# Performance work log

Measured on AMD Instinct MI355X. Metric: run time of the kernel, lower is better.

The kernel has to match this reference:

```python
import jax, jax.numpy as jnp
import numpy as np

N_NODES, N_LAYERS, D = 4096, 8, 128


def setup_inputs() -> dict:
    key = jax.random.key(0)
    k1, k2, k3 = jax.random.split(key, 3)
    feature = jax.random.normal(k1, (N_NODES, N_LAYERS, D), dtype=jnp.float32)
    W = jax.random.uniform(k2, (D, D), dtype=jnp.float32)
    adj = jax.random.randint(k3, (N_LAYERS, N_NODES, N_NODES), 0, 2, dtype=jnp.int32)
    return {"feature": feature, "W": W, "adj": adj}


def reference(feature, W, adj):
    # feature: [N, L, D]; W: [D, D]; adj: [L, N, N] with 0/1 entries.
    # Original loop: for i, for l, for j in neighbors(i) U {i}:
    #     ret[j, l, :] = (W @ feature[i, l, :]) / sqrt(d_i * d_j)   # OVERWRITE
    # => final ret[j, l] uses the LAST source i with adj[l,i,j]==1 or i==j.
    L, N = adj.shape[0], adj.shape[1]
    i_idx = jnp.arange(N)
    # mask[l, i, j]: source i writes to destination j at layer l
    mask = (adj == 1) | (i_idx[:, None] == i_idx[None, :])
    # last (largest) source index per (l, j); diagonal guarantees >= 0
    src = jnp.max(jnp.where(mask, i_idx[:, None], -1), axis=1)          # [L, N]
    deg = jnp.sum(adj, axis=2).astype(feature.dtype) + 1.0              # [L, N]
    # shared tiny GEMM applied to all (node, layer) features
    Wf = jnp.einsum('de,nle->lnd', W, feature)                          # [L, N, D]
    gathered = jnp.take_along_axis(Wf, src[:, :, None], axis=1)         # [L, N, D]
    d_src = jnp.take_along_axis(deg, src, axis=1)                       # [L, N]
    scale = 1.0 / jnp.sqrt(d_src * deg)                                 # [L, N]
    ret = jnp.transpose(gathered * scale[:, :, None], (1, 0, 2))        # [N, L, D]
    return ret
```

## Files before the change

kernel.cpp:

```cpp
#include <hip/hip_runtime.h>
#include <cstddef>

#define NN 4096
#define NL 8
#define ND 128

#define CHUNK 64
#define BATCH 16

typedef int   int4v   __attribute__((ext_vector_type(4)));
typedef float float4v __attribute__((ext_vector_type(4)));

__global__ __launch_bounds__(512, 4) void fused_kernel(
    const float* __restrict__ feature, const float* __restrict__ W,
    const int* __restrict__ adj, float* __restrict__ out) {
  __shared__ int      s_cand[32][CHUNK];
  __shared__ int      s_src[CHUNK];
  __shared__ int      s_found[CHUNK];
  __shared__ unsigned s_mask[NN / 32];
  __shared__ int      s_ps[NN / 32];
  __shared__ int      s_list[CHUNK];
  __shared__ int      s_smap[CHUNK];
  __shared__ float    s_scj[CHUNK];
  __shared__ float    s_deg[2 * CHUNK];
  __shared__ float    s_fb[BATCH][ND];
  __shared__ float    s_wf[BATCH][ND];

  const int t = threadIdx.x;
  const int l = blockIdx.y;
  const int jbase = blockIdx.x * CHUNK;
  const int* __restrict__ Al = adj + (size_t)l * NN * NN;

  if (t < CHUNK) { s_src[t] = jbase + t; s_found[t] = 0; }
  if (t < NN / 32) s_mask[t] = 0u;
  __syncthreads();

  const int rw = t >> 4;
  const int cq = t & 15;
  int itop = NN - 1;
  for (;;) {
    const int i = itop - rw;
    int4v a = {0, 0, 0, 0};
    if (i > jbase)
      a = *reinterpret_cast<const int4v*>(Al + (size_t)i * NN + jbase + cq * 4);
    int4v c;
    c.x = (a.x != 0 && i > jbase + cq * 4 + 0) ? i : -1;
    c.y = (a.y != 0 && i > jbase + cq * 4 + 1) ? i : -1;
    c.z = (a.z != 0 && i > jbase + cq * 4 + 2) ? i : -1;
    c.w = (a.w != 0 && i > jbase + cq * 4 + 3) ? i : -1;
    *reinterpret_cast<int4v*>(&s_cand[rw][cq * 4]) = c;
    __syncthreads();
    bool mydone = true;
    if (t < CHUNK) {
      if (!s_found[t]) {
        int best = -1;
#pragma unroll
        for (int k = 0; k < 32; ++k) best = max(best, s_cand[k][t]);
        if (best >= 0) { s_src[t] = best; s_found[t] = 1; }
      }
      mydone = s_found[t] || (itop - 32 <= jbase + t);
    }
    itop -= 32;
    if (__syncthreads_and((int)mydone) || itop < 0) break;
  }

  if (t < CHUNK) atomicOr(&s_mask[s_src[t] >> 5], 1u << (s_src[t] & 31));
  __syncthreads();
  int pc = 0;
  if (t < 128) { pc = __popc(s_mask[t]); s_ps[t] = pc; }
  __syncthreads();
  for (int off = 1; off < 128; off <<= 1) {
    int v = 0;
    if (t < 128 && t >= off) v = s_ps[t - off];
    __syncthreads();
    if (t < 128 && t >= off) s_ps[t] += v;
    __syncthreads();
  }
  if (t < 128) {
    unsigned m = s_mask[t];
    int pos = s_ps[t] - pc;
    while (m) {
      int b = __ffs(m) - 1;
      m &= m - 1;
      s_list[pos++] = (t << 5) | b;
    }
  }
  __syncthreads();
  const int cnt = s_ps[127];
  if (t < CHUNK) {
    const int v = s_src[t], w = v >> 5;
    const int base = (w > 0) ? s_ps[w - 1] : 0;
    s_smap[t] = base + __popc(s_mask[w] & ((1u << (v & 31)) - 1));
  }

  const int wv = t >> 6;
  const int lane = t & 63;
  for (int r = wv; r < CHUNK; r += 8) {
    const int row = jbase + r;
    const int4v* __restrict__ p =
        reinterpret_cast<const int4v*>(Al + (size_t)row * NN);
    int s = 0;
    if (row & 1) {
#pragma unroll
      for (int k = 0; k < 16; ++k) {
        int4v v = __builtin_nontemporal_load(&p[lane + k * 64]);
        s += v.x + v.y + v.z + v.w;
      }
    } else {
#pragma unroll
      for (int k = 0; k < 16; ++k) {
        int4v v = p[lane + k * 64];
        s += v.x + v.y + v.z + v.w;
      }
    }
    for (int off = 32; off > 0; off >>= 1) s += __shfl_down(s, off, 64);
    if (lane == 0) s_deg[r] = (float)s + 1.0f;
  }
  for (int r = wv; r < cnt; r += 8) {
    const int4v* __restrict__ p =
        reinterpret_cast<const int4v*>(Al + (size_t)s_list[r] * NN);
    int s = 0;
#pragma unroll
    for (int k = 0; k < 16; ++k) {
      int4v v = p[lane + k * 64];
      s += v.x + v.y + v.z + v.w;
    }
    for (int off = 32; off > 0; off >>= 1) s += __shfl_down(s, off, 64);
    if (lane == 0) s_deg[CHUNK + r] = (float)s + 1.0f;
  }
  __syncthreads();
  if (t < CHUNK)
    s_scj[t] = rsqrtf(s_deg[t] * s_deg[CHUNK + s_smap[t]]);

  const int d = t & 127;
  const int quarter = t >> 7;
  const float4v* __restrict__ Wd =
      reinterpret_cast<const float4v*>(W + (size_t)d * ND);

  for (int b0 = 0; b0 < cnt; b0 += BATCH) {
    const int nb = min(BATCH, cnt - b0);
    {
      const int k = t >> 5, q = t & 31;
      if (k < nb)
        reinterpret_cast<float4v*>(s_fb[k])[q] =
            reinterpret_cast<const float4v*>(
                feature + ((size_t)s_list[b0 + k] * NL + l) * ND)[q];
    }
    __syncthreads();

#pragma unroll
    for (int kk = 0; kk < 4; ++kk) {
      const int k = quarter * 4 + kk;
      if (k < nb) {
        float4v a4 = {0.f, 0.f, 0.f, 0.f};
#pragma unroll
        for (int q = 0; q < 32; ++q)
          a4 += Wd[q] * reinterpret_cast<const float4v*>(s_fb[k])[q];
        s_wf[k][d] = a4.x + a4.y + a4.z + a4.w;
      }
    }
    __syncthreads();

    for (int idx = t; idx < CHUNK * 32; idx += 512) {
      const int r = idx >> 5, q = idx & 31;
      const int sl = s_smap[r] - b0;
      if (sl >= 0 && sl < nb) {
        const float sc = s_scj[r];
        float4v v = reinterpret_cast<const float4v*>(s_wf[sl])[q];
        v.x *= sc; v.y *= sc; v.z *= sc; v.w *= sc;
        __builtin_nontemporal_store(
            v, reinterpret_cast<float4v*>(out) +
                   ((size_t)(jbase + r) * NL + l) * 32 + q);
      }
    }
    __syncthreads();
  }
}

extern "C" void kernel_launch(void* const* d_in, const int* in_sizes, int n_in,
                              void* d_out, int out_size, void* d_ws,
                              size_t ws_size, hipStream_t stream) {
  const float* feature = (const float*)d_in[0];
  const float* W       = (const float*)d_in[1];
  const int*   adj     = (const int*)d_in[2];
  float* out = (float*)d_out;

  fused_kernel<<<dim3(NN / CHUNK, NL), 512, 0, stream>>>(feature, W, adj, out);
}
```

Measured before the change: 113.0 us.

## Overlap source search with degree row sums via warp specialization

Doubles the destination chunk per block and splits the block's waves into roles. Seven waves compute destination-row degree sums. The eighth wave alone scans the adjacency columns top-down with scalar loads to find the last source, builds the compacted source list with a wave-level scan, sums the source rows' degrees, and preloads the first feature batch. The goal is to hide the serialized search and its many block barriers behind the bandwidth-bound row-sum reads. The cost is that one wave now does the search and all source-row sums serially with strided scalar loads, and grid parallelism is halved.

```diff
diff --git a/kernel.cpp b/kernel.cpp
--- a/kernel.cpp
+++ b/kernel.cpp
@@ -5,18 +5,16 @@
 #define NL 8
 #define ND 128
 
-#define CHUNK 64
+#define CHUNK 128
 #define BATCH 16
 
 typedef int   int4v   __attribute__((ext_vector_type(4)));
 typedef float float4v __attribute__((ext_vector_type(4)));
 
-__global__ __launch_bounds__(512, 4) void fused_kernel(
+__global__ __launch_bounds__(512, 2) void fused_kernel(
     const float* __restrict__ feature, const float* __restrict__ W,
     const int* __restrict__ adj, float* __restrict__ out) {
-  __shared__ int      s_cand[32][CHUNK];
   __shared__ int      s_src[CHUNK];
-  __shared__ int      s_found[CHUNK];
   __shared__ unsigned s_mask[NN / 32];
   __shared__ int      s_ps[NN / 32];
   __shared__ int      s_list[CHUNK];
@@ -30,105 +28,125 @@
   const int l = blockIdx.y;
   const int jbase = blockIdx.x * CHUNK;
   const int* __restrict__ Al = adj + (size_t)l * NN * NN;
-
-  if (t < CHUNK) { s_src[t] = jbase + t; s_found[t] = 0; }
-  if (t < NN / 32) s_mask[t] = 0u;
-  __syncthreads();
-
-  const int rw = t >> 4;
-  const int cq = t & 15;
-  int itop = NN - 1;
-  for (;;) {
-    const int i = itop - rw;
-    int4v a = {0, 0, 0, 0};
-    if (i > jbase)
-      a = *reinterpret_cast<const int4v*>(Al + (size_t)i * NN + jbase + cq * 4);
-    int4v c;
-    c.x = (a.x != 0 && i > jbase + cq * 4 + 0) ? i : -1;
-    c.y = (a.y != 0 && i > jbase + cq * 4 + 1) ? i : -1;
-    c.z = (a.z != 0 && i > jbase + cq * 4 + 2) ? i : -1;
-    c.w = (a.w != 0 && i > jbase + cq * 4 + 3) ? i : -1;
-    *reinterpret_cast<int4v*>(&s_cand[rw][cq * 4]) = c;
-    __syncthreads();
-    bool mydone = true;
-    if (t < CHUNK) {
-      if (!s_found[t]) {
-        int best = -1;
-#pragma unroll
-        for (int k = 0; k < 32; ++k) best = max(best, s_cand[k][t]);
-        if (best >= 0) { s_src[t] = best; s_found[t] = 1; }
-      }
-      mydone = s_found[t] || (itop - 32 <= jbase + t);
-    }
-    itop -= 32;
-    if (__syncthreads_and((int)mydone) || itop < 0) break;
-  }
-
-  if (t < CHUNK) atomicOr(&s_mask[s_src[t] >> 5], 1u << (s_src[t] & 31));
-  __syncthreads();
-  int pc = 0;
-  if (t < 128) { pc = __popc(s_mask[t]); s_ps[t] = pc; }
-  __syncthreads();
-  for (int off = 1; off < 128; off <<= 1) {
-    int v = 0;
-    if (t < 128 && t >= off) v = s_ps[t - off];
-    __syncthreads();
-    if (t < 128 && t >= off) s_ps[t] += v;
-    __syncthreads();
-  }
-  if (t < 128) {
-    unsigned m = s_mask[t];
-    int pos = s_ps[t] - pc;
-    while (m) {
-      int b = __ffs(m) - 1;
-      m &= m - 1;
-      s_list[pos++] = (t << 5) | b;
-    }
-  }
-  __syncthreads();
-  const int cnt = s_ps[127];
-  if (t < CHUNK) {
-    const int v = s_src[t], w = v >> 5;
-    const int base = (w > 0) ? s_ps[w - 1] : 0;
-    s_smap[t] = base + __popc(s_mask[w] & ((1u << (v & 31)) - 1));
-  }
-
   const int wv = t >> 6;
   const int lane = t & 63;
-  for (int r = wv; r < CHUNK; r += 8) {
-    const int row = jbase + r;
-    const int4v* __restrict__ p =
-        reinterpret_cast<const int4v*>(Al + (size_t)row * NN);
-    int s = 0;
-    if (row & 1) {
-#pragma unroll
-      for (int k = 0; k < 16; ++k) {
-        int4v v = __builtin_nontemporal_load(&p[lane + k * 64]);
-        s += v.x + v.y + v.z + v.w;
-      }
-    } else {
+
+  if (wv < 7) {
+    for (int r = wv; r < CHUNK; r += 7) {
+      const int row = jbase + r;
+      const int4v* __restrict__ p =
+          reinterpret_cast<const int4v*>(Al + (size_t)row * NN);
+      int s = 0;
+      if (row & 1) {
+#pragma unroll
+        for (int k = 0; k < 16; ++k) {
+          int4v v = __builtin_nontemporal_load(&p[lane + k * 64]);
+          s += v.x + v.y + v.z + v.w;
+        }
+      } else {
+#pragma unroll
+        for (int k = 0; k < 16; ++k) {
+          int4v v = p[lane + k * 64];
+          s += v.x + v.y + v.z + v.w;
+        }
+      }
+      for (int off = 32; off > 0; off >>= 1) s += __shfl_down(s, off, 64);
+      if (lane == 0) s_deg[r] = (float)s + 1.0f;
+    }
+  } else {
+    const int j0 = jbase + lane;
+    const int j1 = jbase + 64 + lane;
+    int src0 = j0, src1 = j1;
+    bool f0 = false, f1 = false;
+    int itop = NN - 1;
+    for (;;) {
+      int a0[8], a1[8];
+#pragma unroll
+      for (int r = 0; r < 8; ++r) {
+        const int i = itop - r;
+        a0[r] = (i > j0) ? Al[(size_t)i * NN + j0] : 0;
+        a1[r] = (i > j1) ? Al[(size_t)i * NN + j1] : 0;
+      }
+#pragma unroll
+      for (int r = 0; r < 8; ++r) {
+        const int i = itop - r;
+        if (!f0 && a0[r] != 0 && i > j0) { src0 = i; f0 = true; }
+        if (!f1 && a1[r] != 0 && i > j1) { src1 = i; f1 = true; }
+      }
+      itop -= 8;
+      if (__all((f0 || itop <= j0) && (f1 || itop <= j1))) break;
+    }
+    s_src[lane] = src0;
+    s_src[lane + 64] = src1;
+    s_mask[2 * lane] = 0u;
+    s_mask[2 * lane + 1] = 0u;
+    __threadfence_block();
+    atomicOr(&s_mask[src0 >> 5], 1u << (src0 & 31));
+    atomicOr(&s_mask[src1 >> 5], 1u << (src1 & 31));
+    __threadfence_block();
+
+    const unsigned m0 = s_mask[2 * lane];
+    const unsigned m1 = s_mask[2 * lane + 1];
+    const int c = __popc(m0) + __popc(m1);
+    int sc = c;
+    for (int off = 1; off < 64; off <<= 1) {
+      int v = __shfl_up(sc, off, 64);
+      if (lane >= off) sc += v;
+    }
+    const int excl = sc - c;
+    const int ps0 = excl + __popc(m0);
+    s_ps[2 * lane] = ps0;
+    s_ps[2 * lane + 1] = ps0 + __popc(m1);
+    int pos = excl;
+    unsigned mm = m0;
+    while (mm) {
+      const int b = __ffs(mm) - 1;
+      mm &= mm - 1;
+      s_list[pos++] = ((2 * lane) << 5) | b;
+    }
+    mm = m1;
+    while (mm) {
+      const int b = __ffs(mm) - 1;
+      mm &= mm - 1;
+      s_list[pos++] = ((2 * lane + 1) << 5) | b;
+    }
+    const int cnt = __shfl(sc, 63, 64);
+    __threadfence_block();
+    {
+      const int v = src0, w = v >> 5;
+      const int base = (w > 0) ? s_ps[w - 1] : 0;
+      s_smap[lane] = base + __popc(s_mask[w] & ((1u << (v & 31)) - 1));
+    }
+    {
+      const int v = src1, w = v >> 5;
+      const int base = (w > 0) ? s_ps[w - 1] : 0;
+      s_smap[lane + 64] = base + __popc(s_mask[w] & ((1u << (v & 31)) - 1));
+    }
+    __threadfence_block();
+    for (int r = 0; r < cnt; ++r) {
+      const int4v* __restrict__ p =
+          reinterpret_cast<const int4v*>(Al + (size_t)s_list[r] * NN);
+      int s = 0;
 #pragma unroll
       for (int k = 0; k < 16; ++k) {
         int4v v = p[lane + k * 64];
         s += v.x + v.y + v.z + v.w;
       }
-    }
-    for (int off = 32; off > 0; off >>= 1) s += __shfl_down(s, off, 64);
-    if (lane == 0) s_deg[r] = (float)s + 1.0f;
-  }
-  for (int r = wv; r < cnt; r += 8) {
-    const int4v* __restrict__ p =
-        reinterpret_cast<const int4v*>(Al + (size_t)s_list[r] * NN);
-    int s = 0;
-#pragma unroll
-    for (int k = 0; k < 16; ++k) {
-      int4v v = p[lane + k * 64];
-      s += v.x + v.y + v.z + v.w;
-    }
-    for (int off = 32; off > 0; off >>= 1) s += __shfl_down(s, off, 64);
-    if (lane == 0) s_deg[CHUNK + r] = (float)s + 1.0f;
+      for (int off = 32; off > 0; off >>= 1) s += __shfl_down(s, off, 64);
+      if (lane == 0) s_deg[CHUNK + r] = (float)s + 1.0f;
+    }
+    const int nb0 = min(cnt, BATCH);
+    for (int idx = lane; idx < nb0 * 32; idx += 64) {
+      const int k = idx >> 5, q = idx & 31;
+      reinterpret_cast<float4v*>(s_fb[k])[q] =
+          reinterpret_cast<const float4v*>(
+              feature + ((size_t)s_list[k] * NL + l) * ND)[q];
+    }
   }
   __syncthreads();
+
+  const int cnt = s_ps[127];
+  const int nb0 = min(cnt, BATCH);
   if (t < CHUNK)
     s_scj[t] = rsqrtf(s_deg[t] * s_deg[CHUNK + s_smap[t]]);
 
@@ -136,18 +154,42 @@
   const int quarter = t >> 7;
   const float4v* __restrict__ Wd =
       reinterpret_cast<const float4v*>(W + (size_t)d * ND);
-
-  for (int b0 = 0; b0 < cnt; b0 += BATCH) {
+#pragma unroll
+  for (int kk = 0; kk < 4; ++kk) {
+    const int k = quarter * 4 + kk;
+    if (k < nb0) {
+      float4v a4 = {0.f, 0.f, 0.f, 0.f};
+#pragma unroll
+      for (int q = 0; q < 32; ++q)
+        a4 += Wd[q] * reinterpret_cast<const float4v*>(s_fb[k])[q];
+      s_wf[k][d] = a4.x + a4.y + a4.z + a4.w;
+    }
+  }
+  __syncthreads();
+
+  for (int idx = t; idx < CHUNK * 32; idx += 512) {
+    const int r = idx >> 5, q = idx & 31;
+    const int sl = s_smap[r];
+    if (sl < nb0) {
+      const float sc = s_scj[r];
+      float4v v = reinterpret_cast<const float4v*>(s_wf[sl])[q];
+      v.x *= sc; v.y *= sc; v.z *= sc; v.w *= sc;
+      __builtin_nontemporal_store(
+          v, reinterpret_cast<float4v*>(out) +
+                 ((size_t)(jbase + r) * NL + l) * 32 + q);
+    }
+  }
+
+  for (int b0 = BATCH; b0 < cnt; b0 += BATCH) {
     const int nb = min(BATCH, cnt - b0);
-    {
-      const int k = t >> 5, q = t & 31;
-      if (k < nb)
-        reinterpret_cast<float4v*>(s_fb[k])[q] =
-            reinterpret_cast<const float4v*>(
-                feature + ((size_t)s_list[b0 + k] * NL + l) * ND)[q];
-    }
     __syncthreads();
-
+    for (int idx = t; idx < nb * 32; idx += 512) {
+      const int k = idx >> 5, q = idx & 31;
+      reinterpret_cast<float4v*>(s_fb[k])[q] =
+          reinterpret_cast<const float4v*>(
+              feature + ((size_t)s_list[b0 + k] * NL + l) * ND)[q];
+    }
+    __syncthreads();
 #pragma unroll
     for (int kk = 0; kk < 4; ++kk) {
       const int k = quarter * 4 + kk;
@@ -160,7 +202,6 @@
       }
     }
     __syncthreads();
-
     for (int idx = t; idx < CHUNK * 32; idx += 512) {
       const int r = idx >> 5, q = idx & 31;
       const int sl = s_smap[r] - b0;
@@ -173,7 +214,6 @@
                    ((size_t)(jbase + r) * NL + l) * 32 + q);
       }
     }
-    __syncthreads();
   }
 }
 
```

Result: slower. 115.3 us (+2.1%).
